# Kernel tuning notes

Measured on AMD Instinct MI355X. Metric: run time of the kernel, lower is better.

The kernel has to match this reference:

```python
import jax, jax.numpy as jnp
import numpy as np

D_MODEL = 1024
NUM_HEADS = 16
HEAD_DIM = D_MODEL // NUM_HEADS
THETA = 10000.0


def _init_linear(key, d_out, d_in):
    sigma = np.sqrt(2.0 / (d_in + d_out))
    w = jax.random.truncated_normal(key, -3.0, 3.0, (d_out, d_in), dtype=jnp.float32)
    return w * sigma


def setup_inputs() -> dict:
    key = jax.random.key(0)
    kh, kq, kk, kv, ko = jax.random.split(key, 5)
    h = jax.random.normal(kh, (2, 2048, D_MODEL), dtype=jnp.float32)
    return {
        "h": h,
        "wq": _init_linear(kq, D_MODEL, D_MODEL),
        "wk": _init_linear(kk, D_MODEL, D_MODEL),
        "wv": _init_linear(kv, D_MODEL, D_MODEL),
        "wo": _init_linear(ko, D_MODEL, D_MODEL),
    }


def _rope(x, pos):
    # x: [B, H, T, dh]; rotate interleaved pairs (..., 2k, 2k+1)
    dh = x.shape[-1]
    freq = THETA ** (-jnp.arange(0, dh // 2, dtype=jnp.float32) / (dh // 2))
    ang = pos[:, None] * freq[None, :]            # [T, dh/2]
    cos, sin = jnp.cos(ang), jnp.sin(ang)
    xr = x.reshape(*x.shape[:-1], dh // 2, 2)
    x0, x1 = xr[..., 0], xr[..., 1]
    out = jnp.stack((cos * x0 - sin * x1, sin * x0 + cos * x1), axis=-1)
    return out.reshape(x.shape)


def reference(h, wq, wk, wv, wo):
    B, T, D = h.shape
    Hn, dh = NUM_HEADS, HEAD_DIM

    def split_heads(x):  # [B,T,D] -> [B,H,T,dh]
        return x.reshape(B, T, Hn, dh).transpose(0, 2, 1, 3)

    Q = split_heads(h @ wq.T)
    K = split_heads(h @ wk.T)
    V = split_heads(h @ wv.T)

    pos = jnp.arange(T, dtype=jnp.float32)
    Q = _rope(Q, pos)
    K = _rope(K, pos)

    scores = jnp.einsum('bhqd,bhkd->bhqk', Q, K) / jnp.sqrt(jnp.float32(dh))
    mask = jnp.tril(jnp.ones((T, T), dtype=bool))
    scores = jnp.where(mask, scores, -jnp.inf)
    attn = jax.nn.softmax(scores, axis=-1)
    out = jnp.einsum('bhqk,bhkd->bhqd', attn, V)   # [B,H,T,dh]
    out = out.transpose(0, 2, 1, 3).reshape(B, T, D)
    return out @ wo.T
```

## Files before the change

### kernel.cpp

```cpp
#include <hip/hip_runtime.h>
#include <math.h>

typedef __bf16 bf16_t;
typedef __bf16 v8bf __attribute__((ext_vector_type(8)));
typedef __bf16 v4bf __attribute__((ext_vector_type(4)));
typedef float  v4f  __attribute__((ext_vector_type(4)));

#define AS1 __attribute__((address_space(1)))
#define AS3 __attribute__((address_space(3)))

static __device__ __forceinline__ void load_lds16(const bf16_t* g, bf16_t* l) {
    __builtin_amdgcn_global_load_lds((AS1 void*)const_cast<bf16_t*>(g),
                                     (AS3 void*)l, 16, 0, 0);
}

static __device__ __forceinline__ void fast_sincos(float ang, float* sn, float* cs) {
    float rv = ang * 0.15915494309189535f;
    rv -= floorf(rv);
    const float a = rv * 6.283185307179586f;
    *sn = __sinf(a);
    *cs = __cosf(a);
}

__global__ __launch_bounds__(256) void cvt_fp32_bf16(
    const float* __restrict__ h,  const float* __restrict__ wq,
    const float* __restrict__ wk, const float* __restrict__ wv,
    const float* __restrict__ wo,
    bf16_t* __restrict__ hb,  bf16_t* __restrict__ wqb,
    bf16_t* __restrict__ wkb, bf16_t* __restrict__ wvb,
    bf16_t* __restrict__ wob)
{
    const size_t HM = (size_t)4 << 20;
    const size_t i8 = ((size_t)blockIdx.x * 256 + threadIdx.x) * 8;
    const float* src; bf16_t* dst; size_t off;
    if (i8 < HM) { src = h; dst = hb; off = i8; }
    else {
        const size_t r = (i8 - HM) >> 20;
        off = (i8 - HM) & (((size_t)1 << 20) - 1);
        src = (r == 0) ? wq  : (r == 1) ? wk  : (r == 2) ? wv  : wo;
        dst = (r == 0) ? wqb : (r == 1) ? wkb : (r == 2) ? wvb : wob;
    }
    const float4 a = *(const float4*)(src + off);
    const float4 b = *(const float4*)(src + off + 4);
    v8bf o;
    o[0]=(bf16_t)a.x; o[1]=(bf16_t)a.y; o[2]=(bf16_t)a.z; o[3]=(bf16_t)a.w;
    o[4]=(bf16_t)b.x; o[5]=(bf16_t)b.y; o[6]=(bf16_t)b.z; o[7]=(bf16_t)b.w;
    *(v8bf*)(dst + off) = o;
}

__global__ __launch_bounds__(256) void qkv_gemm_rope(
    const bf16_t* __restrict__ A,
    const bf16_t* __restrict__ wq,
    const bf16_t* __restrict__ wk,
    const bf16_t* __restrict__ wv,
    bf16_t* __restrict__ qo, bf16_t* __restrict__ ko, bf16_t* __restrict__ vo)
{
    __shared__ __align__(16) bf16_t smem[17408];
    bf16_t* As = smem;
    bf16_t* Bs = smem + 4096;

    const int tid = threadIdx.x;
    const int n0  = blockIdx.x * 128;
    const int m0  = blockIdx.y * 128;
    const int sel = n0 >> 10;
    const bf16_t* W = (sel == 0) ? wq : (sel == 1) ? wk : wv;
    const int wr0 = n0 & 1023;

    const int wave = tid >> 6;
    const int lane = tid & 63;
    const int l16  = lane & 15;
    const int quad = lane >> 4;
    const int wrow = (wave >> 1) * 64;
    const int wcol = (wave & 1) * 64;

    v4f acc[4][4];
    #pragma unroll
    for (int i = 0; i < 4; ++i)
        #pragma unroll
        for (int j = 0; j < 4; ++j) acc[i][j] = (v4f)(0.0f);

    for (int kt = 0; kt < 32; ++kt) {
        const int k0 = kt * 32;
        #pragma unroll
        for (int rep = 0; rep < 2; ++rep) {
            const int c   = rep * 256 + tid;
            const int row = c >> 2;
            const int col = (c & 3) * 8;
            load_lds16(A + (size_t)(m0 + row) * 1024 + k0 + col, &As[c * 8]);
            load_lds16(W + (size_t)(wr0 + row) * 1024 + k0 + col, &Bs[c * 8]);
        }
        __syncthreads();

        v8bf af[4], bfb[4];
        #pragma unroll
        for (int i = 0; i < 4; ++i) {
            af[i]  = *(const v8bf*)&As[(wrow + i * 16 + l16) * 32 + quad * 8];
            bfb[i] = *(const v8bf*)&Bs[(wcol + i * 16 + l16) * 32 + quad * 8];
        }
        #pragma unroll
        for (int i = 0; i < 4; ++i)
            #pragma unroll
            for (int j = 0; j < 4; ++j)
                acc[i][j] = __builtin_amdgcn_mfma_f32_16x16x32_bf16(
                    af[i], bfb[j], acc[i][j], 0, 0, 0);
        __syncthreads();
    }

    bf16_t* Ls = smem + wave * 4352;
    const int bq     = (m0 + wrow) >> 11;
    const int hd     = ((n0 + wcol) >> 6) & 15;
    const int t_base = (m0 + wrow) & 2047;

    if (sel < 2) {
        bf16_t* OUT = (sel == 0) ? qo : ko;
        #pragma unroll
        for (int i = 0; i < 4; ++i) {
            #pragma unroll
            for (int j = 0; j < 4; ++j) {
                #pragma unroll
                for (int r = 0; r < 4; ++r) {
                    const int mrow = i * 16 + quad * 4 + r;
                    const int dcol = j * 16 + l16;
                    float v = acc[i][j][r];
                    const float vp = __shfl_xor(v, 1);
                    const int t  = t_base + mrow;
                    const int kk = dcol >> 1;
                    const float freq = exp2f((float)kk * -0.4152410118609203f);
                    float sn, cs;
                    fast_sincos((float)t * freq, &sn, &cs);
                    v = ((dcol & 1) == 0) ? (cs * v - sn * vp) : (sn * vp + cs * v);
                    Ls[mrow * 68 + dcol] = (bf16_t)v;
                }
            }
        }
        #pragma unroll
        for (int s = 0; s < 8; ++s) {
            const int row = s * 8 + (lane >> 3);
            const int off = (lane & 7) * 8;
            const v8bf vv = *(const v8bf*)&Ls[row * 68 + off];
            *(v8bf*)(OUT + (((size_t)(bq * 16 + hd) * 2048) + t_base + row) * 64 + off) = vv;
        }
    } else {
        #pragma unroll
        for (int i = 0; i < 4; ++i)
            #pragma unroll
            for (int j = 0; j < 4; ++j) {
                v4bf p;
                #pragma unroll
                for (int r = 0; r < 4; ++r) p[r] = (bf16_t)acc[i][j][r];
                *(v4bf*)&Ls[(j * 16 + l16) * 68 + i * 16 + quad * 4] = p;
            }
        #pragma unroll
        for (int s = 0; s < 8; ++s) {
            const int drow = s * 8 + (lane >> 3);
            const int off  = (lane & 7) * 8;
            const v8bf vv = *(const v8bf*)&Ls[drow * 68 + off];
            *(v8bf*)(vo + (((size_t)(bq * 16 + hd) * 64) + drow) * 2048 + t_base + off) = vv;
        }
    }
}

__global__ __launch_bounds__(256, 4) void attn_mfma(
    const bf16_t* __restrict__ qg,
    const bf16_t* __restrict__ kg,
    const bf16_t* __restrict__ vtg,
    bf16_t* __restrict__ og)
{
    __shared__ __align__(16) bf16_t Ks[64 * 72];
    __shared__ __align__(16) bf16_t Ps[4][16 * 72];

    const int tid  = threadIdx.x;
    const int wave = tid >> 6;
    const int lane = tid & 63;
    const int l16  = lane & 15;
    const int quad = lane >> 4;

    const int i  = blockIdx.x;
    const int tt = i >> 3;
    const int u  = tt & 31;
    const int g  = tt >> 5;
    const int qt = (g & 1) ? u : (31 - u);
    const int bh = (i & 7) * 4 + g;
    const int b = bh >> 4, hh = bh & 15;

    const bf16_t* Kb = kg  + (size_t)bh * 2048 * 64;
    const bf16_t* Vb = vtg + (size_t)bh * 64 * 2048;

    const int qglb = qt * 64 + wave * 16 + l16;

    const bf16_t* qrow = qg + ((size_t)bh * 2048 + qglb) * 64;
    v8bf qf[2];
    qf[0] = *(const v8bf*)(qrow + quad * 8);
    qf[1] = *(const v8bf*)(qrow + 32 + quad * 8);
    #pragma unroll
    for (int e = 0; e < 8; ++e) {
        qf[0][e] = (bf16_t)((float)qf[0][e] * 0.18033688011112042f);
        qf[1][e] = (bf16_t)((float)qf[1][e] * 0.18033688011112042f);
    }

    float m_r = -1e30f, l_r = 0.0f;
    v4f o_acc[4];
    #pragma unroll
    for (int d = 0; d < 4; ++d) o_acc[d] = (v4f)(0.0f);

    v8bf kreg[2];
    #pragma unroll
    for (int rep = 0; rep < 2; ++rep) {
        const int c = rep * 256 + tid;
        const int row = c >> 3, col = (c & 7) * 8;
        kreg[rep] = *(const v8bf*)(Kb + (size_t)row * 64 + col);
    }

    for (int kt = 0; kt <= qt; ++kt) {
        __syncthreads();
        #pragma unroll
        for (int rep = 0; rep < 2; ++rep) {
            const int c = rep * 256 + tid;
            const int row = c >> 3, col = (c & 7) * 8;
            *(v8bf*)&Ks[row * 72 + col] = kreg[rep];
        }
        __syncthreads();

        if (kt < qt) {
            #pragma unroll
            for (int rep = 0; rep < 2; ++rep) {
                const int c = rep * 256 + tid;
                const int row = c >> 3, col = (c & 7) * 8;
                kreg[rep] = *(const v8bf*)(Kb + ((size_t)(kt + 1) * 64 + row) * 64 + col);
            }
        }

        v8bf vf[4][2];
        #pragma unroll
        for (int dblk = 0; dblk < 4; ++dblk) {
            const bf16_t* vrow = Vb + (size_t)(dblk * 16 + l16) * 2048 + kt * 64;
            vf[dblk][0] = *(const v8bf*)(vrow + quad * 8);
            vf[dblk][1] = *(const v8bf*)(vrow + 32 + quad * 8);
        }

        v4f s_acc[4];
        #pragma unroll
        for (int kblk = 0; kblk < 4; ++kblk) s_acc[kblk] = (v4f)(0.0f);
        #pragma unroll
        for (int kblk = 0; kblk < 4; ++kblk) {
            const v8bf kf0 = *(const v8bf*)&Ks[(kblk * 16 + l16) * 72 + quad * 8];
            const v8bf kf1 = *(const v8bf*)&Ks[(kblk * 16 + l16) * 72 + 32 + quad * 8];
            s_acc[kblk] = __builtin_amdgcn_mfma_f32_16x16x32_bf16(
                kf0, qf[0], s_acc[kblk], 0, 0, 0);
            s_acc[kblk] = __builtin_amdgcn_mfma_f32_16x16x32_bf16(
                kf1, qf[1], s_acc[kblk], 0, 0, 0);
        }

        if (kt == qt) {
            #pragma unroll
            for (int kblk = 0; kblk < 4; ++kblk)
                #pragma unroll
                for (int r = 0; r < 4; ++r)
                    if (kblk * 16 + quad * 4 + r > wave * 16 + l16)
                        s_acc[kblk][r] = -1e30f;
        }

        float mx = -1e30f;
        #pragma unroll
        for (int kblk = 0; kblk < 4; ++kblk)
            #pragma unroll
            for (int r = 0; r < 4; ++r) mx = fmaxf(mx, s_acc[kblk][r]);
        mx = fmaxf(mx, __shfl_xor(mx, 16));
        mx = fmaxf(mx, __shfl_xor(mx, 32));
        const float m_new = fmaxf(m_r, mx);
        float ssum = 0.0f;
        #pragma unroll
        for (int kblk = 0; kblk < 4; ++kblk)
            #pragma unroll
            for (int r = 0; r < 4; ++r) {
                const float p = exp2f(s_acc[kblk][r] - m_new);
                s_acc[kblk][r] = p;
                ssum += p;
            }
        ssum += __shfl_xor(ssum, 16);
        ssum += __shfl_xor(ssum, 32);
        const float alpha = exp2f(m_r - m_new);
        l_r = l_r * alpha + ssum;
        m_r = m_new;

        #pragma unroll
        for (int kblk = 0; kblk < 4; ++kblk) {
            v4bf p;
            #pragma unroll
            for (int r = 0; r < 4; ++r) p[r] = (bf16_t)s_acc[kblk][r];
            *(v4bf*)&Ps[wave][l16 * 72 + kblk * 16 + quad * 4] = p;
        }
        #pragma unroll
        for (int d = 0; d < 4; ++d) o_acc[d] *= alpha;

        const v8bf pf0 = *(const v8bf*)&Ps[wave][l16 * 72 + quad * 8];
        const v8bf pf1 = *(const v8bf*)&Ps[wave][l16 * 72 + 32 + quad * 8];
        #pragma unroll
        for (int dblk = 0; dblk < 4; ++dblk) {
            o_acc[dblk] = __builtin_amdgcn_mfma_f32_16x16x32_bf16(
                vf[dblk][0], pf0, o_acc[dblk], 0, 0, 0);
            o_acc[dblk] = __builtin_amdgcn_mfma_f32_16x16x32_bf16(
                vf[dblk][1], pf1, o_acc[dblk], 0, 0, 0);
        }
    }

    const float inv_l = 1.0f / l_r;
    const size_t base = ((size_t)b * 2048 + qglb) * 1024 + hh * 64;
    #pragma unroll
    for (int dblk = 0; dblk < 4; ++dblk) {
        v4bf o;
        #pragma unroll
        for (int r = 0; r < 4; ++r) o[r] = (bf16_t)(o_acc[dblk][r] * inv_l);
        *(v4bf*)(og + base + dblk * 16 + quad * 4) = o;
    }
}

__global__ __launch_bounds__(256) void out_gemm(
    const bf16_t* __restrict__ A,
    const bf16_t* __restrict__ W,
    float* __restrict__ C)
{
    __shared__ __align__(16) float smemf[8448];
    bf16_t* As = (bf16_t*)smemf;
    bf16_t* Bs = As + 4096;

    const int tid = threadIdx.x;
    const int n0  = blockIdx.x * 128;
    const int m0  = blockIdx.y * 128;

    const int wave = tid >> 6;
    const int lane = tid & 63;
    const int l16  = lane & 15;
    const int quad = lane >> 4;
    const int wrow = (wave >> 1) * 64;
    const int wcol = (wave & 1) * 64;

    v4f acc[4][4];
    #pragma unroll
    for (int i = 0; i < 4; ++i)
        #pragma unroll
        for (int j = 0; j < 4; ++j) acc[i][j] = (v4f)(0.0f);

    for (int kt = 0; kt < 32; ++kt) {
        const int k0 = kt * 32;
        #pragma unroll
        for (int rep = 0; rep < 2; ++rep) {
            const int c   = rep * 256 + tid;
            const int row = c >> 2;
            const int col = (c & 3) * 8;
            load_lds16(A + (size_t)(m0 + row) * 1024 + k0 + col, &As[c * 8]);
            load_lds16(W + (size_t)(n0 + row) * 1024 + k0 + col, &Bs[c * 8]);
        }
        __syncthreads();

        v8bf af[4], bfb[4];
        #pragma unroll
        for (int i = 0; i < 4; ++i) {
            af[i]  = *(const v8bf*)&As[(wrow + i * 16 + l16) * 32 + quad * 8];
            bfb[i] = *(const v8bf*)&Bs[(wcol + i * 16 + l16) * 32 + quad * 8];
        }
        #pragma unroll
        for (int i = 0; i < 4; ++i)
            #pragma unroll
            for (int j = 0; j < 4; ++j)
                acc[i][j] = __builtin_amdgcn_mfma_f32_16x16x32_bf16(
                    af[i], bfb[j], acc[i][j], 0, 0, 0);
        __syncthreads();
    }

    float* Lw = smemf + wave * 2112;
    #pragma unroll
    for (int half = 0; half < 2; ++half) {
        #pragma unroll
        for (int ii = 0; ii < 2; ++ii) {
            const int i = half * 2 + ii;
            #pragma unroll
            for (int j = 0; j < 4; ++j)
                #pragma unroll
                for (int r = 0; r < 4; ++r)
                    Lw[(ii * 16 + quad * 4 + r) * 66 + j * 16 + l16] = acc[i][j][r];
        }
        __syncthreads();
        #pragma unroll
        for (int s = 0; s < 16; ++s) {
            const int row = s * 2 + (lane >> 5);
            const int off = (lane & 31) * 2;
            const float2 vv = *(const float2*)&Lw[row * 66 + off];
            *(float2*)(C + (size_t)(m0 + wrow + half * 32 + row) * 1024 + n0 + wcol + off) = vv;
        }
        __syncthreads();
    }
}

extern "C" void kernel_launch(void* const* d_in, const int* in_sizes, int n_in,
                              void* d_out, int out_size, void* d_ws, size_t ws_size,
                              hipStream_t stream) {
    const float* h  = (const float*)d_in[0];
    const float* wq = (const float*)d_in[1];
    const float* wk = (const float*)d_in[2];
    const float* wv = (const float*)d_in[3];
    const float* wo = (const float*)d_in[4];

    const size_t NH = (size_t)4096 * 1024;
    const size_t NW = (size_t)1024 * 1024;

    bf16_t* hb  = (bf16_t*)d_ws;
    bf16_t* wqb = hb  + NH;
    bf16_t* wkb = wqb + NW;
    bf16_t* wvb = wkb + NW;
    bf16_t* wob = wvb + NW;
    bf16_t* qw  = wob + NW;
    bf16_t* kw  = qw + NH;
    bf16_t* vw  = kw + NH;
    bf16_t* og  = hb;

    cvt_fp32_bf16<<<dim3(4096), dim3(256), 0, stream>>>(
        h, wq, wk, wv, wo, hb, wqb, wkb, wvb, wob);
    qkv_gemm_rope<<<dim3(24, 32), dim3(256), 0, stream>>>(
        hb, wqb, wkb, wvb, qw, kw, vw);
    attn_mfma<<<dim3(1024), dim3(256), 0, stream>>>(qw, kw, vw, og);
    out_gemm<<<dim3(8, 32), dim3(256), 0, stream>>>(og, wob, (float*)d_out);
}
```

Baseline: 214.3 us.

## Use 128-query attention blocks with double-buffered K/V in LDS; shrink out-GEMM tile

Result: faster. 187.4 us (-12.6%).

```diff
diff --git a/kernel.cpp b/kernel.cpp
--- a/kernel.cpp
+++ b/kernel.cpp
@@ -160,14 +160,15 @@
     }
 }
 
-__global__ __launch_bounds__(256, 4) void attn_mfma(
+__global__ __launch_bounds__(512, 4) void attn_mfma(
     const bf16_t* __restrict__ qg,
     const bf16_t* __restrict__ kg,
     const bf16_t* __restrict__ vtg,
     bf16_t* __restrict__ og)
 {
-    __shared__ __align__(16) bf16_t Ks[64 * 72];
-    __shared__ __align__(16) bf16_t Ps[4][16 * 72];
+    __shared__ __align__(16) bf16_t Ks[2][64 * 72];
+    __shared__ __align__(16) bf16_t Vs[2][64 * 72];
+    __shared__ __align__(16) bf16_t Ps[8][16 * 72];
 
     const int tid  = threadIdx.x;
     const int wave = tid >> 6;
@@ -177,16 +178,18 @@
 
     const int i  = blockIdx.x;
     const int tt = i >> 3;
-    const int u  = tt & 31;
-    const int g  = tt >> 5;
-    const int qt = (g & 1) ? u : (31 - u);
+    const int u  = tt & 15;
+    const int g  = tt >> 4;
+    const int q128 = (((g + 1) >> 1) & 1) ? (15 - u) : u;
     const int bh = (i & 7) * 4 + g;
     const int b = bh >> 4, hh = bh & 15;
 
     const bf16_t* Kb = kg  + (size_t)bh * 2048 * 64;
     const bf16_t* Vb = vtg + (size_t)bh * 64 * 2048;
 
-    const int qglb = qt * 64 + wave * 16 + l16;
+    const int qglb = q128 * 128 + wave * 16 + l16;
+    const int diag_kt = 2 * q128 + (wave >> 2);
+    const int ktmax = 2 * q128 + 1;
 
     const bf16_t* qrow = qg + ((size_t)bh * 2048 + qglb) * 64;
     v8bf qf[2];
@@ -203,104 +206,99 @@
     #pragma unroll
     for (int d = 0; d < 4; ++d) o_acc[d] = (v4f)(0.0f);
 
-    v8bf kreg[2];
-    #pragma unroll
-    for (int rep = 0; rep < 2; ++rep) {
-        const int c = rep * 256 + tid;
-        const int row = c >> 3, col = (c & 7) * 8;
-        kreg[rep] = *(const v8bf*)(Kb + (size_t)row * 64 + col);
-    }
-
-    for (int kt = 0; kt <= qt; ++kt) {
+    const int srow = tid >> 3;
+    const int scol = (tid & 7) * 8;
+    {
+        const v8bf k0 = *(const v8bf*)(Kb + (size_t)srow * 64 + scol);
+        const v8bf v0 = *(const v8bf*)(Vb + (size_t)srow * 2048 + scol);
+        *(v8bf*)&Ks[0][srow * 72 + scol] = k0;
+        *(v8bf*)&Vs[0][srow * 72 + scol] = v0;
+    }
+
+    for (int kt = 0; kt <= ktmax; ++kt) {
+        const int cur = kt & 1;
+        const int nxt = cur ^ 1;
         __syncthreads();
-        #pragma unroll
-        for (int rep = 0; rep < 2; ++rep) {
-            const int c = rep * 256 + tid;
-            const int row = c >> 3, col = (c & 7) * 8;
-            *(v8bf*)&Ks[row * 72 + col] = kreg[rep];
-        }
-        __syncthreads();
-
-        if (kt < qt) {
-            #pragma unroll
-            for (int rep = 0; rep < 2; ++rep) {
-                const int c = rep * 256 + tid;
-                const int row = c >> 3, col = (c & 7) * 8;
-                kreg[rep] = *(const v8bf*)(Kb + ((size_t)(kt + 1) * 64 + row) * 64 + col);
-            }
-        }
-
-        v8bf vf[4][2];
-        #pragma unroll
-        for (int dblk = 0; dblk < 4; ++dblk) {
-            const bf16_t* vrow = Vb + (size_t)(dblk * 16 + l16) * 2048 + kt * 64;
-            vf[dblk][0] = *(const v8bf*)(vrow + quad * 8);
-            vf[dblk][1] = *(const v8bf*)(vrow + 32 + quad * 8);
-        }
-
-        v4f s_acc[4];
-        #pragma unroll
-        for (int kblk = 0; kblk < 4; ++kblk) s_acc[kblk] = (v4f)(0.0f);
-        #pragma unroll
-        for (int kblk = 0; kblk < 4; ++kblk) {
-            const v8bf kf0 = *(const v8bf*)&Ks[(kblk * 16 + l16) * 72 + quad * 8];
-            const v8bf kf1 = *(const v8bf*)&Ks[(kblk * 16 + l16) * 72 + 32 + quad * 8];
-            s_acc[kblk] = __builtin_amdgcn_mfma_f32_16x16x32_bf16(
-                kf0, qf[0], s_acc[kblk], 0, 0, 0);
-            s_acc[kblk] = __builtin_amdgcn_mfma_f32_16x16x32_bf16(
-                kf1, qf[1], s_acc[kblk], 0, 0, 0);
-        }
-
-        if (kt == qt) {
+
+        v8bf kreg, vreg;
+        if (kt < ktmax) {
+            kreg = *(const v8bf*)(Kb + ((size_t)(kt + 1) * 64 + srow) * 64 + scol);
+            vreg = *(const v8bf*)(Vb + (size_t)srow * 2048 + (kt + 1) * 64 + scol);
+        }
+
+        const bool active = (kt * 64) <= (q128 * 128 + wave * 16 + 15);
+        if (active) {
+            v4f s_acc[4];
+            #pragma unroll
+            for (int kblk = 0; kblk < 4; ++kblk) s_acc[kblk] = (v4f)(0.0f);
+            #pragma unroll
+            for (int kblk = 0; kblk < 4; ++kblk) {
+                const v8bf kf0 = *(const v8bf*)&Ks[cur][(kblk * 16 + l16) * 72 + quad * 8];
+                const v8bf kf1 = *(const v8bf*)&Ks[cur][(kblk * 16 + l16) * 72 + 32 + quad * 8];
+                s_acc[kblk] = __builtin_amdgcn_mfma_f32_16x16x32_bf16(
+                    kf0, qf[0], s_acc[kblk], 0, 0, 0);
+                s_acc[kblk] = __builtin_amdgcn_mfma_f32_16x16x32_bf16(
+                    kf1, qf[1], s_acc[kblk], 0, 0, 0);
+            }
+
+            if (kt == diag_kt) {
+                #pragma unroll
+                for (int kblk = 0; kblk < 4; ++kblk)
+                    #pragma unroll
+                    for (int r = 0; r < 4; ++r)
+                        if (kt * 64 + kblk * 16 + quad * 4 + r > qglb)
+                            s_acc[kblk][r] = -1e30f;
+            }
+
+            float mx = -1e30f;
             #pragma unroll
             for (int kblk = 0; kblk < 4; ++kblk)
                 #pragma unroll
-                for (int r = 0; r < 4; ++r)
-                    if (kblk * 16 + quad * 4 + r > wave * 16 + l16)
-                        s_acc[kblk][r] = -1e30f;
-        }
-
-        float mx = -1e30f;
-        #pragma unroll
-        for (int kblk = 0; kblk < 4; ++kblk)
-            #pragma unroll
-            for (int r = 0; r < 4; ++r) mx = fmaxf(mx, s_acc[kblk][r]);
-        mx = fmaxf(mx, __shfl_xor(mx, 16));
-        mx = fmaxf(mx, __shfl_xor(mx, 32));
-        const float m_new = fmaxf(m_r, mx);
-        float ssum = 0.0f;
-        #pragma unroll
-        for (int kblk = 0; kblk < 4; ++kblk)
-            #pragma unroll
-            for (int r = 0; r < 4; ++r) {
-                const float p = exp2f(s_acc[kblk][r] - m_new);
-                s_acc[kblk][r] = p;
-                ssum += p;
-            }
-        ssum += __shfl_xor(ssum, 16);
-        ssum += __shfl_xor(ssum, 32);
-        const float alpha = exp2f(m_r - m_new);
-        l_r = l_r * alpha + ssum;
-        m_r = m_new;
-
-        #pragma unroll
-        for (int kblk = 0; kblk < 4; ++kblk) {
-            v4bf p;
-            #pragma unroll
-            for (int r = 0; r < 4; ++r) p[r] = (bf16_t)s_acc[kblk][r];
-            *(v4bf*)&Ps[wave][l16 * 72 + kblk * 16 + quad * 4] = p;
-        }
-        #pragma unroll
-        for (int d = 0; d < 4; ++d) o_acc[d] *= alpha;
-
-        const v8bf pf0 = *(const v8bf*)&Ps[wave][l16 * 72 + quad * 8];
-        const v8bf pf1 = *(const v8bf*)&Ps[wave][l16 * 72 + 32 + quad * 8];
-        #pragma unroll
-        for (int dblk = 0; dblk < 4; ++dblk) {
-            o_acc[dblk] = __builtin_amdgcn_mfma_f32_16x16x32_bf16(
-                vf[dblk][0], pf0, o_acc[dblk], 0, 0, 0);
-            o_acc[dblk] = __builtin_amdgcn_mfma_f32_16x16x32_bf16(
-                vf[dblk][1], pf1, o_acc[dblk], 0, 0, 0);
+                for (int r = 0; r < 4; ++r) mx = fmaxf(mx, s_acc[kblk][r]);
+            mx = fmaxf(mx, __shfl_xor(mx, 16));
+            mx = fmaxf(mx, __shfl_xor(mx, 32));
+            const float m_new = fmaxf(m_r, mx);
+            float ssum = 0.0f;
+            #pragma unroll
+            for (int kblk = 0; kblk < 4; ++kblk)
+                #pragma unroll
+                for (int r = 0; r < 4; ++r) {
+                    const float p = exp2f(s_acc[kblk][r] - m_new);
+                    s_acc[kblk][r] = p;
+                    ssum += p;
+                }
+            ssum += __shfl_xor(ssum, 16);
+            ssum += __shfl_xor(ssum, 32);
+            const float alpha = exp2f(m_r - m_new);
+            l_r = l_r * alpha + ssum;
+            m_r = m_new;
+
+            #pragma unroll
+            for (int kblk = 0; kblk < 4; ++kblk) {
+                v4bf p;
+                #pragma unroll
+                for (int r = 0; r < 4; ++r) p[r] = (bf16_t)s_acc[kblk][r];
+                *(v4bf*)&Ps[wave][l16 * 72 + kblk * 16 + quad * 4] = p;
+            }
+            #pragma unroll
+            for (int d = 0; d < 4; ++d) o_acc[d] *= alpha;
+
+            const v8bf pf0 = *(const v8bf*)&Ps[wave][l16 * 72 + quad * 8];
+            const v8bf pf1 = *(const v8bf*)&Ps[wave][l16 * 72 + 32 + quad * 8];
+            #pragma unroll
+            for (int dblk = 0; dblk < 4; ++dblk) {
+                const v8bf vf0 = *(const v8bf*)&Vs[cur][(dblk * 16 + l16) * 72 + quad * 8];
+                const v8bf vf1 = *(const v8bf*)&Vs[cur][(dblk * 16 + l16) * 72 + 32 + quad * 8];
+                o_acc[dblk] = __builtin_amdgcn_mfma_f32_16x16x32_bf16(
+                    vf0, pf0, o_acc[dblk], 0, 0, 0);
+                o_acc[dblk] = __builtin_amdgcn_mfma_f32_16x16x32_bf16(
+                    vf1, pf1, o_acc[dblk], 0, 0, 0);
+            }
+        }
+
+        if (kt < ktmax) {
+            *(v8bf*)&Ks[nxt][srow * 72 + scol] = kreg;
+            *(v8bf*)&Vs[nxt][srow * 72 + scol] = vreg;
         }
     }
 
@@ -320,12 +318,12 @@
     const bf16_t* __restrict__ W,
     float* __restrict__ C)
 {
-    __shared__ __align__(16) float smemf[8448];
+    __shared__ __align__(16) float smemf[4352];
     bf16_t* As = (bf16_t*)smemf;
     bf16_t* Bs = As + 4096;
 
     const int tid = threadIdx.x;
-    const int n0  = blockIdx.x * 128;
+    const int n0  = blockIdx.x * 64;
     const int m0  = blockIdx.y * 128;
 
     const int wave = tid >> 6;
@@ -333,13 +331,13 @@
     const int l16  = lane & 15;
     const int quad = lane >> 4;
     const int wrow = (wave >> 1) * 64;
-    const int wcol = (wave & 1) * 64;
-
-    v4f acc[4][4];
+    const int wcol = (wave & 1) * 32;
+
+    v4f acc[4][2];
     #pragma unroll
     for (int i = 0; i < 4; ++i)
         #pragma unroll
-        for (int j = 0; j < 4; ++j) acc[i][j] = (v4f)(0.0f);
+        for (int j = 0; j < 2; ++j) acc[i][j] = (v4f)(0.0f);
 
     for (int kt = 0; kt < 32; ++kt) {
         const int k0 = kt * 32;
@@ -349,46 +347,49 @@
             const int row = c >> 2;
             const int col = (c & 3) * 8;
             load_lds16(A + (size_t)(m0 + row) * 1024 + k0 + col, &As[c * 8]);
-            load_lds16(W + (size_t)(n0 + row) * 1024 + k0 + col, &Bs[c * 8]);
+        }
+        {
+            const int row = tid >> 2;
+            const int col = (tid & 3) * 8;
+            load_lds16(W + (size_t)(n0 + row) * 1024 + k0 + col, &Bs[tid * 8]);
         }
         __syncthreads();
 
-        v8bf af[4], bfb[4];
-        #pragma unroll
-        for (int i = 0; i < 4; ++i) {
+        v8bf af[4], bfb[2];
+        #pragma unroll
+        for (int i = 0; i < 4; ++i)
             af[i]  = *(const v8bf*)&As[(wrow + i * 16 + l16) * 32 + quad * 8];
-            bfb[i] = *(const v8bf*)&Bs[(wcol + i * 16 + l16) * 32 + quad * 8];
-        }
+        #pragma unroll
+        for (int j = 0; j < 2; ++j)
+            bfb[j] = *(const v8bf*)&Bs[(wcol + j * 16 + l16) * 32 + quad * 8];
         #pragma unroll
         for (int i = 0; i < 4; ++i)
             #pragma unroll
-            for (int j = 0; j < 4; ++j)
+            for (int j = 0; j < 2; ++j)
                 acc[i][j] = __builtin_amdgcn_mfma_f32_16x16x32_bf16(
                     af[i], bfb[j], acc[i][j], 0, 0, 0);
         __syncthreads();
     }
 
-    float* Lw = smemf + wave * 2112;
+    float* Lw = smemf + wave * 1088;
     #pragma unroll
     for (int half = 0; half < 2; ++half) {
         #pragma unroll
         for (int ii = 0; ii < 2; ++ii) {
             const int i = half * 2 + ii;
             #pragma unroll
-            for (int j = 0; j < 4; ++j)
+            for (int j = 0; j < 2; ++j)
                 #pragma unroll
                 for (int r = 0; r < 4; ++r)
-                    Lw[(ii * 16 + quad * 4 + r) * 66 + j * 16 + l16] = acc[i][j][r];
-        }
-        __syncthreads();
-        #pragma unroll
-        for (int s = 0; s < 16; ++s) {
-            const int row = s * 2 + (lane >> 5);
-            const int off = (lane & 31) * 2;
-            const float2 vv = *(const float2*)&Lw[row * 66 + off];
-            *(float2*)(C + (size_t)(m0 + wrow + half * 32 + row) * 1024 + n0 + wcol + off) = vv;
-        }
-        __syncthreads();
+                    Lw[(ii * 16 + quad * 4 + r) * 34 + j * 16 + l16] = acc[i][j][r];
+        }
+        #pragma unroll
+        for (int s = 0; s < 8; ++s) {
+            const int row = s * 4 + (lane >> 4);
+            const float2 vv = *(const float2*)&Lw[row * 34 + l16 * 2];
+            *(float2*)(C + (size_t)(m0 + wrow + half * 32 + row) * 1024
+                         + n0 + wcol + l16 * 2) = vv;
+        }
     }
 }
 
@@ -418,6 +419,6 @@
         h, wq, wk, wv, wo, hb, wqb, wkb, wvb, wob);
     qkv_gemm_rope<<<dim3(24, 32), dim3(256), 0, stream>>>(
         hb, wqb, wkb, wvb, qw, kw, vw);
-    attn_mfma<<<dim3(1024), dim3(256), 0, stream>>>(qw, kw, vw, og);
-    out_gemm<<<dim3(8, 32), dim3(256), 0, stream>>>(og, wob, (float*)d_out);
-}
+    attn_mfma<<<dim3(512), dim3(512), 0, stream>>>(qw, kw, vw, og);
+    out_gemm<<<dim3(16, 32), dim3(256), 0, stream>>>(og, wob, (float*)d_out);
+}
```
